# Performance work log

Hardware: AMD Instinct MI355X
Metric: run time of the kernel (lower is better)

The kernel has to match this reference:

```python
import jax, jax.numpy as jnp
import numpy as np

X_DIM = 64
N_FREQ = 16


def setup_inputs() -> dict:
    key = jax.random.key(0)
    k1, k2 = jax.random.split(key)
    z = jax.random.normal(k1, (32, 2 * X_DIM * N_FREQ), dtype=jnp.float32)
    x_q = jax.random.normal(k2, (32, 4096, X_DIM), dtype=jnp.float32)
    return {"z": z, "x_q": x_q}


def reference(z, x_q):
    b = z.shape[0]
    # split z into amplitudes and frequencies, each [b, d, f]
    amplitudes, freqs = jnp.split(z, 2, axis=-1)
    amplitudes = amplitudes.reshape(b, X_DIM, N_FREQ)
    freqs = freqs.reshape(b, X_DIM, N_FREQ)
    # [b,q,d,f] sinusoidal features
    x = jnp.sin(jnp.einsum('bqd,bdf->bqdf', x_q, freqs))
    # contract over d,f -> [b,q]
    y = jnp.einsum('bqdf,bdf->bq', x, amplitudes)
    return y[..., None]
```

## Files before the change

kernel.cpp:

```cpp
#include <hip/hip_runtime.h>
#include <hip/hip_fp16.h>

#define ND 64
#define NF 16
#define TPTS 512
#define SEGP 16
#define DELTA 0.03125f
#define XSCALE 32.0f
#define XBIAS 256.0f
#define IMAX 510.99f
#define DSL 32
#define QSL 512

__global__ __launch_bounds__(256) void sinreg_build(
    const float* __restrict__ z, unsigned* __restrict__ tblg, int B) {
  const int t = blockIdx.x * 256 + threadIdx.x;
  const int b   = t >> 11;
  const int d   = (t >> 5) & (ND - 1);
  const int seg = t & 31;
  const int k0  = seg * SEGP;
  const float xs = -8.0f + k0 * DELTA;

  const float* __restrict__ zb = z + (size_t)b * (2 * ND * NF);
  const float* __restrict__ ap = zb + d * NF;
  const float* __restrict__ fp = zb + ND * NF + d * NF;
  constexpr float INV2PI = 0.15915494309189535f;

  float g[SEGP + 1];
  #pragma unroll
  for (int k = 0; k <= SEGP; ++k) g[k] = 0.f;

  #pragma unroll
  for (int f = 0; f < NF; ++f) {
    const float fv = fp[f], av = ap[f];
    float s0 = __builtin_amdgcn_sinf(__builtin_amdgcn_fractf(fv * xs * INV2PI));
    float s1 = __builtin_amdgcn_sinf(
        __builtin_amdgcn_fractf(fv * (xs + DELTA) * INV2PI));
    const float th2 = (fv * DELTA) * (fv * DELTA);
    const float w = fmaf(th2, fmaf(th2, 0.0833333333f, -1.0f), 2.0f);
    g[0] = fmaf(av, s0, g[0]);
    g[1] = fmaf(av, s1, g[1]);
    #pragma unroll
    for (int k = 2; k <= SEGP; ++k) {
      const float s2 = fmaf(w, s1, -s0);
      g[k] = fmaf(av, s2, g[k]);
      s0 = s1; s1 = s2;
    }
  }

  unsigned pk[SEGP];
  #pragma unroll
  for (int k = 0; k < SEGP; ++k) {
    __half2 h;
    h.x = __float2half(g[k]);
    h.y = __float2half(g[k + 1] - g[k]);
    pk[k] = *reinterpret_cast<unsigned*>(&h);
  }
  uint4* __restrict__ dst =
      reinterpret_cast<uint4*>(tblg + ((size_t)(b * ND + d) * TPTS) + k0);
  #pragma unroll
  for (int j = 0; j < 4; ++j)
    dst[j] = make_uint4(pk[4 * j], pk[4 * j + 1], pk[4 * j + 2], pk[4 * j + 3]);
}

__global__ __launch_bounds__(512, 4) void sinreg_lookup(
    const unsigned* __restrict__ tblg,
    const float* __restrict__ xq,
    float* __restrict__ out,
    int B, int Q) {
  __shared__ unsigned s_tbl[DSL * TPTS];

  const int b   = blockIdx.y;
  const int dsl = blockIdx.x & 1;
  const int qsl = blockIdx.x >> 1;
  const int tid = threadIdx.x;

  {
    const uint4* __restrict__ src =
        reinterpret_cast<const uint4*>(tblg + (size_t)(b * ND + dsl * DSL) * TPTS);
    uint4* __restrict__ dst = reinterpret_cast<uint4*>(s_tbl);
    #pragma unroll
    for (int i = 0; i < 8; ++i) dst[tid + i * 512] = src[tid + i * 512];
  }
  __syncthreads();

  const int lane = tid & 63;
  const int wv   = tid >> 6;
  const int qsub = lane >> 4;
  const int dp   = (lane & 15) * 2;

  const unsigned* __restrict__ trow0 = &s_tbl[dp * TPTS];
  const unsigned* __restrict__ trow1 = trow0 + TPTS;

  const int qw0 = qsl * QSL + wv * 64;
  const float* __restrict__ xbase =
      xq + ((size_t)b * Q + qw0 + qsub) * ND + dsl * DSL + dp;

  #pragma unroll 4
  for (int it = 0; it < 16; ++it) {
    const float2 x2 = *reinterpret_cast<const float2*>(xbase + (size_t)it * 4 * ND);

    float r;
    {
      float tt = fmaf(x2.x, XSCALE, XBIAS);
      tt = fminf(fmaxf(tt, 0.0f), IMAX);
      const unsigned i = (unsigned)tt;
      const float u = tt - (float)i;
      const unsigned pv = trow0[i];
      const float2 gs = __half22float2(*reinterpret_cast<const __half2*>(&pv));
      r = fmaf(gs.y, u, gs.x);
    }
    {
      float tt = fmaf(x2.y, XSCALE, XBIAS);
      tt = fminf(fmaxf(tt, 0.0f), IMAX);
      const unsigned i = (unsigned)tt;
      const float u = tt - (float)i;
      const unsigned pv = trow1[i];
      const float2 gs = __half22float2(*reinterpret_cast<const __half2*>(&pv));
      r = fmaf(gs.y, u, gs.x + r);
    }
    r += __shfl_xor(r, 1);
    r += __shfl_xor(r, 2);
    r += __shfl_xor(r, 4);
    r += __shfl_xor(r, 8);
    if ((lane & 15) == 0)
      atomicAdd(&out[(size_t)b * Q + qw0 + it * 4 + qsub], r);
  }
}

__global__ __launch_bounds__(256, 4) void sinreg_direct(
    const float* __restrict__ z, const float* __restrict__ xq,
    float* __restrict__ out, int B, int Q) {
  __shared__ float s_part[4][64];
  const int b = blockIdx.y;
  const int lane = threadIdx.x & 63;
  const int wv = __builtin_amdgcn_readfirstlane((int)(threadIdx.x >> 6));
  const int q = blockIdx.x * 64 + lane;
  const float* __restrict__ zb  = z + (size_t)b * (2 * ND * NF);
  const float* __restrict__ amp = zb + (16 * wv) * NF;
  const float* __restrict__ frq = zb + ND * NF + (16 * wv) * NF;
  const float4* __restrict__ xrow =
      reinterpret_cast<const float4*>(xq + ((size_t)b * Q + q) * ND + 16 * wv);
  float4 xv0 = xrow[0], xv1 = xrow[1], xv2 = xrow[2], xv3 = xrow[3];
  constexpr float INV2PI = 0.15915494309189535f;
  const float xs[16] = {
      xv0.x * INV2PI, xv0.y * INV2PI, xv0.z * INV2PI, xv0.w * INV2PI,
      xv1.x * INV2PI, xv1.y * INV2PI, xv1.z * INV2PI, xv1.w * INV2PI,
      xv2.x * INV2PI, xv2.y * INV2PI, xv2.z * INV2PI, xv2.w * INV2PI,
      xv3.x * INV2PI, xv3.y * INV2PI, xv3.z * INV2PI, xv3.w * INV2PI};
  float acc0 = 0.f, acc1 = 0.f, acc2 = 0.f, acc3 = 0.f;
  #pragma unroll
  for (int dd = 0; dd < 16; ++dd) {
    const float xsd = xs[dd];
    #pragma unroll
    for (int f = 0; f < NF; f += 4) {
      acc0 = fmaf(__builtin_amdgcn_sinf(__builtin_amdgcn_fractf(xsd * frq[dd * NF + f + 0])), amp[dd * NF + f + 0], acc0);
      acc1 = fmaf(__builtin_amdgcn_sinf(__builtin_amdgcn_fractf(xsd * frq[dd * NF + f + 1])), amp[dd * NF + f + 1], acc1);
      acc2 = fmaf(__builtin_amdgcn_sinf(__builtin_amdgcn_fractf(xsd * frq[dd * NF + f + 2])), amp[dd * NF + f + 2], acc2);
      acc3 = fmaf(__builtin_amdgcn_sinf(__builtin_amdgcn_fractf(xsd * frq[dd * NF + f + 3])), amp[dd * NF + f + 3], acc3);
    }
  }
  s_part[wv][lane] = (acc0 + acc1) + (acc2 + acc3);
  __syncthreads();
  if (threadIdx.x < 64) {
    float r = (s_part[0][lane] + s_part[1][lane]) + (s_part[2][lane] + s_part[3][lane]);
    out[(size_t)b * Q + (size_t)blockIdx.x * 64 + lane] = r;
  }
}

extern "C" void kernel_launch(void* const* d_in, const int* in_sizes, int n_in,
                              void* d_out, int out_size, void* d_ws, size_t ws_size,
                              hipStream_t stream) {
  const float* z  = (const float*)d_in[0];
  const float* xq = (const float*)d_in[1];
  float* out = (float*)d_out;

  const int B = in_sizes[0] / (2 * ND * NF);
  const int Q = in_sizes[1] / (B * ND);

  const size_t tbl_bytes = (size_t)B * ND * TPTS * sizeof(unsigned);
  if (ws_size < tbl_bytes) {
    dim3 grid(Q / 64, B);
    sinreg_direct<<<grid, 256, 0, stream>>>(z, xq, out, B, Q);
    return;
  }

  unsigned* tblg = (unsigned*)d_ws;

  sinreg_build<<<dim3((B * ND * 32) / 256), 256, 0, stream>>>(z, tblg, B);

  hipMemsetAsync(d_out, 0, (size_t)out_size * sizeof(float), stream);

  dim3 grid(2 * (Q / QSL), B);
  sinreg_lookup<<<grid, 512, 0, stream>>>(tblg, xq, out, B, Q);
}
```

Baseline: 25.89 us.

## Process both d-halves per block and drop memset and atomics

Each lookup block now loads the two 32-row halves of the table into shared memory one after the other and keeps partial sums in registers. It then writes the output directly instead of using atomicAdd, so the hipMemsetAsync launch goes away. The q-slice per block is halved so the grid size stays the same. The cost is a second table staging pass per block plus extra barriers, and the second table load is not overlapped with compute.

```diff
diff --git a/kernel.cpp b/kernel.cpp
--- a/kernel.cpp
+++ b/kernel.cpp
@@ -9,8 +9,7 @@
 #define XSCALE 32.0f
 #define XBIAS 256.0f
 #define IMAX 510.99f
-#define DSL 32
-#define QSL 512
+#define QSL 256
 
 __global__ __launch_bounds__(256) void sinreg_build(
     const float* __restrict__ z, unsigned* __restrict__ tblg, int B) {
@@ -68,64 +67,83 @@
     const float* __restrict__ xq,
     float* __restrict__ out,
     int B, int Q) {
-  __shared__ unsigned s_tbl[DSL * TPTS];
+  __shared__ unsigned s_tbl[32 * TPTS];
 
   const int b   = blockIdx.y;
-  const int dsl = blockIdx.x & 1;
-  const int qsl = blockIdx.x >> 1;
+  const int qsl = blockIdx.x;
   const int tid = threadIdx.x;
-
-  {
-    const uint4* __restrict__ src =
-        reinterpret_cast<const uint4*>(tblg + (size_t)(b * ND + dsl * DSL) * TPTS);
-    uint4* __restrict__ dst = reinterpret_cast<uint4*>(s_tbl);
-    #pragma unroll
-    for (int i = 0; i < 8; ++i) dst[tid + i * 512] = src[tid + i * 512];
-  }
-  __syncthreads();
-
   const int lane = tid & 63;
   const int wv   = tid >> 6;
   const int qsub = lane >> 4;
   const int dp   = (lane & 15) * 2;
 
+  const int q0 = qsl * QSL + wv * 32;
   const unsigned* __restrict__ trow0 = &s_tbl[dp * TPTS];
   const unsigned* __restrict__ trow1 = trow0 + TPTS;
 
-  const int qw0 = qsl * QSL + wv * 64;
-  const float* __restrict__ xbase =
-      xq + ((size_t)b * Q + qw0 + qsub) * ND + dsl * DSL + dp;
-
-  #pragma unroll 4
-  for (int it = 0; it < 16; ++it) {
-    const float2 x2 = *reinterpret_cast<const float2*>(xbase + (size_t)it * 4 * ND);
-
-    float r;
-    {
-      float tt = fmaf(x2.x, XSCALE, XBIAS);
-      tt = fminf(fmaxf(tt, 0.0f), IMAX);
-      const unsigned i = (unsigned)tt;
-      const float u = tt - (float)i;
-      const unsigned pv = trow0[i];
-      const float2 gs = __half22float2(*reinterpret_cast<const __half2*>(&pv));
-      r = fmaf(gs.y, u, gs.x);
-    }
-    {
-      float tt = fmaf(x2.y, XSCALE, XBIAS);
-      tt = fminf(fmaxf(tt, 0.0f), IMAX);
-      const unsigned i = (unsigned)tt;
-      const float u = tt - (float)i;
-      const unsigned pv = trow1[i];
-      const float2 gs = __half22float2(*reinterpret_cast<const __half2*>(&pv));
-      r = fmaf(gs.y, u, gs.x + r);
-    }
-    r += __shfl_xor(r, 1);
-    r += __shfl_xor(r, 2);
-    r += __shfl_xor(r, 4);
-    r += __shfl_xor(r, 8);
-    if ((lane & 15) == 0)
-      atomicAdd(&out[(size_t)b * Q + qw0 + it * 4 + qsub], r);
-  }
+  float acc[8];
+
+#define STAGE(H)                                                               \
+  {                                                                            \
+    const uint4* __restrict__ src = reinterpret_cast<const uint4*>(            \
+        tblg + (size_t)(b * ND + (H) * 32) * TPTS);                            \
+    uint4* __restrict__ dst = reinterpret_cast<uint4*>(s_tbl);                 \
+    _Pragma("unroll")                                                          \
+    for (int i = 0; i < 8; ++i) dst[tid + i * 512] = src[tid + i * 512];       \
+  }
+
+#define LOOKUP2(R, XPTR)                                                       \
+  {                                                                            \
+    const float2 x2 = *reinterpret_cast<const float2*>(XPTR);                  \
+    float tt = fmaf(x2.x, XSCALE, XBIAS);                                      \
+    tt = fminf(fmaxf(tt, 0.0f), IMAX);                                         \
+    unsigned i = (unsigned)tt;                                                 \
+    float u = tt - (float)i;                                                   \
+    unsigned pv = trow0[i];                                                    \
+    float2 gs = __half22float2(*reinterpret_cast<const __half2*>(&pv));        \
+    R = fmaf(gs.y, u, gs.x);                                                   \
+    tt = fmaf(x2.y, XSCALE, XBIAS);                                            \
+    tt = fminf(fmaxf(tt, 0.0f), IMAX);                                         \
+    i = (unsigned)tt;                                                          \
+    u = tt - (float)i;                                                         \
+    pv = trow1[i];                                                             \
+    gs = __half22float2(*reinterpret_cast<const __half2*>(&pv));               \
+    R = fmaf(gs.y, u, gs.x + R);                                               \
+    R += __shfl_xor(R, 1);                                                     \
+    R += __shfl_xor(R, 2);                                                     \
+    R += __shfl_xor(R, 4);                                                     \
+    R += __shfl_xor(R, 8);                                                     \
+  }
+
+  STAGE(0);
+  __syncthreads();
+  {
+    const float* __restrict__ xp =
+        xq + ((size_t)b * Q + q0 + qsub) * ND + dp;
+    #pragma unroll
+    for (int it = 0; it < 8; ++it) {
+      float r;
+      LOOKUP2(r, xp + (size_t)it * 4 * ND);
+      acc[it] = r;
+    }
+  }
+  __syncthreads();
+
+  STAGE(1);
+  __syncthreads();
+  {
+    const float* __restrict__ xp =
+        xq + ((size_t)b * Q + q0 + qsub) * ND + 32 + dp;
+    #pragma unroll
+    for (int it = 0; it < 8; ++it) {
+      float r;
+      LOOKUP2(r, xp + (size_t)it * 4 * ND);
+      if ((lane & 15) == 0)
+        out[(size_t)b * Q + q0 + it * 4 + qsub] = acc[it] + r;
+    }
+  }
+#undef STAGE
+#undef LOOKUP2
 }
 
 __global__ __launch_bounds__(256, 4) void sinreg_direct(
@@ -189,8 +207,6 @@
 
   sinreg_build<<<dim3((B * ND * 32) / 256), 256, 0, stream>>>(z, tblg, B);
 
-  hipMemsetAsync(d_out, 0, (size_t)out_size * sizeof(float), stream);
-
-  dim3 grid(2 * (Q / QSL), B);
+  dim3 grid(Q / QSL, B);
   sinreg_lookup<<<grid, 512, 0, stream>>>(tblg, xq, out, B, Q);
 }
```

Result: faster. 25.22 us (-2.6%).
